# Kernel tuning notes

Hardware: AMD Instinct MI355X
Metric: run time of the kernel (lower is better)

## Reference

```python
import jax, jax.numpy as jnp
import numpy as np

B, N, D, R, E = 512, 32, 300, 5, 256
V_SENSE, V_GLOBAL = 20000, 50000  # last_idx_senses, last_idx_globals - last_idx_senses


def setup_inputs() -> dict:
    key = jax.random.key(0)
    ks = jax.random.split(key, 10)
    x = jax.random.normal(ks[0], (B, N, D), jnp.float32)
    edge_index = jax.random.randint(ks[1], (B, 2, E), 0, N)
    edge_type = jnp.sort(jax.random.randint(ks[2], (B, E), 0, R), axis=-1)
    # parameters (xavier-ish scales)
    conv_W = jax.random.normal(ks[3], (R, D, D), jnp.float32) * np.float32(1.0 / np.sqrt(D))
    W0 = jax.random.normal(ks[4], (D, D), jnp.float32) * np.float32(np.sqrt(2.0 / (D + D)))
    update_gate = jnp.ones((1,), jnp.float32)
    glob_W = jax.random.normal(ks[5], (V_GLOBAL, D), jnp.float32) * np.float32(1.0 / np.sqrt(D))
    glob_b = jnp.zeros((V_GLOBAL,), jnp.float32)
    sense_W = jax.random.normal(ks[6], (V_SENSE, D), jnp.float32) * np.float32(1.0 / np.sqrt(D))
    sense_b = jnp.zeros((V_SENSE,), jnp.float32)
    memory0 = jnp.zeros((N, D), jnp.float32)  # initial persisted memory (zeros vector broadcast)
    return dict(x=x, edge_index=edge_index, edge_type=edge_type, conv_W=conv_W, W0=W0,
                update_gate=update_gate, glob_W=glob_W, glob_b=glob_b,
                sense_W=sense_W, sense_b=sense_b, memory0=memory0)


def reference(x, edge_index, edge_type, conv_W, W0, update_gate, glob_W, glob_b, sense_W, sense_b, memory0):
    R_ = conv_W.shape[0]
    N_ = x.shape[1]

    def step(mem, inp):
        xs, ei, et = inp                      # [N,D], [2,E], [E]
        src, dst = ei[0], ei[1]
        # per-relation transformed features (GCNConv, bias=False)
        xw = jnp.einsum('nd,rde->rne', xs, conv_W)          # [R,N,D]
        # per-relation degrees with self-loops (PyG GCNConv symmetric norm)
        onehot = jax.nn.one_hot(et, R_, dtype=xs.dtype)     # [E,R]
        deg = 1.0 + jax.ops.segment_sum(onehot, dst, num_segments=N_)  # [N,R]
        dinv = jax.lax.rsqrt(deg)                           # [N,R]
        coeff = dinv[src, et] * dinv[dst, et]               # [E]
        msg = coeff[:, None] * xw[et, src]                  # [E,D]
        agg = jax.ops.segment_sum(msg, dst, num_segments=N_)  # sum over relations' convs
        self_term = jnp.einsum('rnd,nr->nd', xw, dinv * dinv)  # self-loop of each GCNConv
        composite = agg + self_term
        # prevlayer_connection = eye(N) @ (x @ W_0) = x @ W_0
        proposed = composite + xs @ W0
        new_mem = update_gate * proposed + (1.0 - update_gate) * mem  # rgcn_conv, persisted
        x1 = jax.nn.relu(new_mem)[0]                        # current node features [D]
        return new_mem, x1

    _, x1_all = jax.lax.scan(step, memory0, (x, edge_index, edge_type))  # [B,D]
    logits_g = x1_all @ glob_W.T + glob_b                   # [B,V_GLOBAL]
    logits_s = x1_all @ sense_W.T + sense_b                 # [B,V_SENSE]
    return (jax.nn.log_softmax(logits_g, axis=-1), jax.nn.log_softmax(logits_s, axis=-1))
```

## Files before the change

kernel.cpp:

```cpp
#include <hip/hip_runtime.h>
#include <stdint.h>

#define BDIM   512
#define NNODE  32
#define DDIM   300
#define NREL   5
#define NEDGE  256
#define VGLOB  50000
#define VSENSE 20000

#define K1PAD  1856
#define K2PAD  320
#define TG_GLOB  391
#define TG_SENSE 157
#define TGTOT  548
#define GROWS  50048
#define SROWS  20096
#define WROWS  70144
#define NCHUNK 3
#define KCH    10
#define NSCH   16
#define SCHL   32

#define NB_W2  5480
#define NB_Z   512
#define NB_W   2784

typedef __attribute__((ext_vector_type(8))) short short8;
typedef __attribute__((ext_vector_type(4))) float f32x4;
typedef _Float16 half_t;
typedef __attribute__((ext_vector_type(4))) _Float16 h16x4;

__device__ __forceinline__ unsigned short f2bf(float x) {
    unsigned int u = __float_as_uint(x);
    u += 0x7fffu + ((u >> 16) & 1u);
    return (unsigned short)(u >> 16);
}

__device__ __forceinline__ float powi(float x, int n) {
    float r = 1.f, p = x;
    while (n) { if (n & 1) r *= p; p *= p; n >>= 1; }
    return r;
}

#define AS1 __attribute__((address_space(1)))
#define AS3 __attribute__((address_space(3)))
__device__ __forceinline__ void gload16(const void* gp, void* lp) {
    __builtin_amdgcn_global_load_lds((AS1 void*)gp, (AS3 void*)lp, 16, 0, 0);
}

__global__ __launch_bounds__(256) void k_prep_all(
    const float* __restrict__ x, const int* __restrict__ ei,
    const int* __restrict__ et, unsigned short* __restrict__ Zb,
    const float* __restrict__ convW, const float* __restrict__ W0f,
    unsigned short* __restrict__ Wcb,
    const float* __restrict__ globW, const float* __restrict__ senseW,
    unsigned short* __restrict__ Wgb, int zbase)
{
    int blk = blockIdx.x, t = threadIdx.x;

    if (blk < zbase) {
        int idx = blk * 256 + t;
        int row = idx / 20, q0 = (idx - row * 20) * 4;
        const float* srcp = nullptr;
        if (row < GROWS) { if (row < VGLOB) srcp = globW + (size_t)row * DDIM; }
        else { int sr = row - GROWS; if (sr < VSENSE) srcp = senseW + (size_t)sr * DDIM; }
        unsigned int pk[8];
#pragma unroll
        for (int j = 0; j < 4; j++) {
            int kq = (q0 + j) * 4;
            unsigned int p0 = 0, p1 = 0;
            if (srcp && kq < DDIM) {
                float4 v = *(const float4*)(srcp + kq);
                p0 = (unsigned int)f2bf(v.x) | ((unsigned int)f2bf(v.y) << 16);
                p1 = (unsigned int)f2bf(v.z) | ((unsigned int)f2bf(v.w) << 16);
            }
            pk[2 * j] = p0; pk[2 * j + 1] = p1;
        }
        uint4* dst = (uint4*)(Wgb + (size_t)row * K2PAD + q0 * 4);
        uint4 u0; u0.x = pk[0]; u0.y = pk[1]; u0.z = pk[2]; u0.w = pk[3];
        uint4 u1; u1.x = pk[4]; u1.y = pk[5]; u1.z = pk[6]; u1.w = pk[7];
        dst[0] = u0; dst[1] = u1;
        return;
    }

    if (blk < zbase + NB_Z) {
        int b = blk - zbase;
        __shared__ int   cnt[NNODE * NREL];
        __shared__ float dinv[NNODE * NREL];
        __shared__ int   ssrc[NEDGE];
        __shared__ int   sdst[NEDGE];
        __shared__ int   setp[NEDGE];
        __shared__ float z[6][DDIM];

        const int* src = ei + (size_t)b * 2 * NEDGE;
        const int* dst = src + NEDGE;
        const int* etb = et + (size_t)b * NEDGE;

        if (t < NNODE * NREL) cnt[t] = 0;
        __syncthreads();
        if (t < NEDGE) {
            int s = src[t], d = dst[t], r = etb[t];
            ssrc[t] = s; sdst[t] = d; setp[t] = r;
            atomicAdd(&cnt[d * NREL + r], 1);
        }
        __syncthreads();
        if (t < NNODE * NREL) dinv[t] = rsqrtf(1.0f + (float)cnt[t]);
        __syncthreads();

        const float* xb = x + (size_t)b * NNODE * DDIM;
        for (int d = t; d < DDIM; d += 256) {
            float x0 = xb[d];
#pragma unroll
            for (int r = 0; r < NREL; r++) { float c = dinv[r]; z[r][d] = c * c * x0; }
            z[5][d] = x0;
        }
        __syncthreads();
        for (int e = 0; e < NEDGE; e++) {
            if (sdst[e] != 0) continue;
            int s = ssrc[e], r = setp[e];
            float coeff = dinv[s * NREL + r] * dinv[r];
            const float* xs = xb + (size_t)s * DDIM;
            for (int d = t; d < DDIM; d += 256) z[r][d] += coeff * xs[d];
        }
        __syncthreads();
        unsigned short* zo = Zb + (size_t)b * K1PAD;
        for (int k = t; k < K1PAD; k += 256) {
            unsigned short v = 0;
            if (k < 6 * DDIM) { int r = k / DDIM, d = k - r * DDIM; v = f2bf(z[r][d]); }
            zo[k] = v;
        }
        return;
    }

    {
        int idx = (blk - zbase - NB_Z) * 256 + t;
        if (idx >= 384 * K1PAD) return;
        int n = idx / K1PAD, k = idx - n * K1PAD;
        float v = 0.f;
        if (n < DDIM && k < 6 * DDIM) {
            int r = k / DDIM, d = k - r * DDIM;
            v = (r < NREL) ? convW[((size_t)r * DDIM + d) * DDIM + n]
                           : W0f[(size_t)d * DDIM + n];
        }
        Wcb[idx] = f2bf(v);
    }
}

template<int MODE, bool ST16>
__global__ __launch_bounds__(256) void k_gemm_b(
    const unsigned short* __restrict__ A, int ldk, int nk, int kchunk,
    int tiles0,
    const unsigned short* __restrict__ B0, int ldb0,
    const float* __restrict__ bias0, void* __restrict__ C0v, long ldc0,
    int nstore0, int tilebase0,
    const unsigned short* __restrict__ B1, int ldb1,
    const float* __restrict__ bias1, void* __restrict__ C1v, long ldc1,
    int nstore1, int tilebase1,
    float* __restrict__ pmax, float* __restrict__ psum)
{
    __shared__ __align__(16) char Alds[128 * 128];
    __shared__ __align__(16) char Blds[128 * 128];

    int t = threadIdx.x;
    int tile, mrep;
    if constexpr (MODE == 0) {
        tile = blockIdx.x; mrep = blockIdx.y;
    } else {
        int i = blockIdx.x + TGTOT * blockIdx.y;
        if (i < 2176) { int g = i >> 5, r = i & 31; tile = g * 8 + (r & 7); mrep = r >> 3; }
        else          { int j = i - 2176; tile = 544 + (j & 3); mrep = j >> 2; }
    }

    const unsigned short* Bp; const float* bias; void* Coutv;
    long ldc; int ldb, nstore, tileidx, tloc;
    if (tile < tiles0) {
        Bp = B0; bias = bias0; Coutv = C0v; ldc = ldc0;
        ldb = ldb0; nstore = nstore0; tloc = tile; tileidx = tilebase0 + tile;
    } else {
        tloc = tile - tiles0;
        Bp = B1; bias = bias1; Coutv = C1v; ldc = ldc1;
        ldb = ldb1; nstore = nstore1; tileidx = tilebase1 + tloc;
    }
    int n0 = tloc * 128;
    int m0 = mrep * 128;

    int kt_lo = 0, kt_hi = nk >> 6;
    float* Cf = (float*)Coutv;
    if constexpr (MODE == 0) {
        if (kchunk > 0) {
            kt_lo = blockIdx.z * kchunk;
            int hi = kt_lo + kchunk;
            if (hi < kt_hi) kt_hi = hi;
            Cf += (size_t)blockIdx.z * (BDIM * 304);
        }
    }

    int lane = t & 63, wid = t >> 6;
    int wm = wid >> 1, wn = wid & 1;
    int l15 = lane & 15, lq = lane >> 4;

    int trow = t >> 3;
    int sb = ((t & 7) << 4) ^ ((trow & 7) << 4);
    const char* Ag = (const char*)A + (size_t)(m0 + trow) * (ldk * 2) + sb;
    const char* Bg = (const char*)Bp + (size_t)(n0 + trow) * (ldb * 2) + sb;
    char* Al = Alds + t * 16;
    char* Bl = Blds + t * 16;
    size_t a32 = (size_t)32 * (ldk * 2);
    size_t b32 = (size_t)32 * (ldb * 2);

    int sw = (l15 & 7) << 4;
    int aoff0 = (lq * 16) ^ sw;
    int aoff1 = (64 + lq * 16) ^ sw;
    const char* Arow = Alds + (wm * 64 + l15) * 128;
    const char* Brow = Blds + (wn * 64 + l15) * 128;

    f32x4 acc[4][4] = {};

    for (int kt = kt_lo; kt < kt_hi; ++kt) {
        int k0b = kt << 7;
        const char* Agk = Ag + k0b;
        const char* Bgk = Bg + k0b;
#pragma unroll
        for (int c = 0; c < 4; c++) {
            gload16(Agk + c * a32, Al + c * 4096);
            gload16(Bgk + c * b32, Bl + c * 4096);
        }
        __syncthreads();
        short8 afr[4][2], bfr[4][2];
#pragma unroll
        for (int i = 0; i < 4; i++) {
            const char* Ab = Arow + i * (16 * 128);
            const char* Bb = Brow + i * (16 * 128);
            afr[i][0] = *(const short8*)(Ab + aoff0);
            afr[i][1] = *(const short8*)(Ab + aoff1);
            bfr[i][0] = *(const short8*)(Bb + aoff0);
            bfr[i][1] = *(const short8*)(Bb + aoff1);
        }
#pragma unroll
        for (int ks = 0; ks < 2; ks++)
#pragma unroll
            for (int mi = 0; mi < 4; mi++)
#pragma unroll
                for (int ni = 0; ni < 4; ni++)
                    acc[mi][ni] = __builtin_amdgcn_mfma_f32_16x16x32_bf16(
                        afr[mi][ks], bfr[ni][ks], acc[mi][ni], 0, 0, 0);
        __syncthreads();
    }

    if constexpr (MODE == 1) {
        half_t* Ch = (half_t*)Coutv;
        __shared__ float sMax[128][2];
        __shared__ float sSum[128][2];
#pragma unroll
        for (int mi = 0; mi < 4; mi++) {
            int row = m0 + wm * 64 + mi * 16 + lq * 4;
#pragma unroll
            for (int r = 0; r < 4; r++) {
                float vals[4];
                float rowmax = -3.0e38f;
#pragma unroll
                for (int ni = 0; ni < 4; ni++) {
                    int col = n0 + wn * 64 + ni * 16 + l15;
                    float v = -3.0e38f;
                    if (col < nstore) v = acc[mi][ni][r] + bias[col];
                    vals[ni] = v;
                    rowmax = fmaxf(rowmax, v);
                }
#pragma unroll
                for (int ni = 0; ni < 4; ni++) {
                    int col = n0 + wn * 64 + ni * 16 + l15;
                    if (col < nstore) {
                        if constexpr (ST16)
                            Ch[(size_t)(row + r) * ldc + col] = (half_t)vals[ni];
                        else
                            Cf[(size_t)(row + r) * ldc + col] = vals[ni];
                    }
                }
#pragma unroll
                for (int off = 1; off < 16; off <<= 1)
                    rowmax = fmaxf(rowmax, __shfl_xor(rowmax, off, 64));
                float s = 0.f;
#pragma unroll
                for (int ni = 0; ni < 4; ni++) s += __expf(vals[ni] - rowmax);
#pragma unroll
                for (int off = 1; off < 16; off <<= 1) s += __shfl_xor(s, off, 64);
                if (l15 == 0) {
                    int rl = wm * 64 + mi * 16 + lq * 4 + r;
                    sMax[rl][wn] = rowmax; sSum[rl][wn] = s;
                }
            }
        }
        __syncthreads();
        if (t < 128) {
            float ma = sMax[t][0], mb = sMax[t][1];
            float M = fmaxf(ma, mb);
            float S = sSum[t][0] * __expf(ma - M) + sSum[t][1] * __expf(mb - M);
            size_t o = (size_t)tileidx * BDIM + (m0 + t);
            pmax[o] = M; psum[o] = S;
        }
    } else {
#pragma unroll
        for (int mi = 0; mi < 4; mi++) {
            int row = m0 + wm * 64 + mi * 16 + lq * 4;
#pragma unroll
            for (int ni = 0; ni < 4; ni++) {
                int col = n0 + wn * 64 + ni * 16 + l15;
                if (col < 304) {
#pragma unroll
                    for (int r = 0; r < 4; r++)
                        Cf[(size_t)(row + r) * ldc + col] = acc[mi][ni][r];
                }
            }
        }
    }
}

__global__ __launch_bounds__(256) void k_gemm_f32(
    const unsigned short* __restrict__ A, int ldk, int nk,
    int tiles0,
    const float* __restrict__ B0, int ldb0, int ksrc0, int brows0,
    const float* __restrict__ bias0, float* __restrict__ C0, long ldc0,
    int nstore0, int tilebase0,
    const float* __restrict__ B1, int ldb1, int ksrc1, int brows1,
    const float* __restrict__ bias1, float* __restrict__ C1, long ldc1,
    int nstore1, int tilebase1,
    float* __restrict__ pmax, float* __restrict__ psum)
{
    __shared__ __align__(16) short Alds[128 * 32];
    __shared__ __align__(16) short Blds[128 * 32];

    int t = threadIdx.x;
    int bx = blockIdx.x;
    const float* Bsrc; const float* bias; float* Cout;
    long ldc; int ldb, ksrc, brows, nstore, tileidx;
    if (bx < tiles0) {
        Bsrc = B0; bias = bias0; Cout = C0; ldc = ldc0;
        ldb = ldb0; ksrc = ksrc0; brows = brows0; nstore = nstore0;
        tileidx = tilebase0 + bx;
    } else {
        bx -= tiles0;
        Bsrc = B1; bias = bias1; Cout = C1; ldc = ldc1;
        ldb = ldb1; ksrc = ksrc1; brows = brows1; nstore = nstore1;
        tileidx = tilebase1 + bx;
    }
    int n0 = bx * 128;
    int m0 = blockIdx.y * 128;

    int lane = t & 63, wid = t >> 6;
    int wm = wid >> 1, wn = wid & 1;
    int l15 = lane & 15, lq = lane >> 4;

    f32x4 acc[4][4] = {};

    int arow = t >> 1, acol = (t & 1) * 16;
    const unsigned short* aptr = A + (size_t)(m0 + arow) * ldk + acol;
    int brow = t >> 3, bkq = (t & 7) * 4;

    int kt_hi = nk / 32;
    for (int kt = 0; kt < kt_hi; ++kt) {
        int k0 = kt * 32;
        uint4 a0 = *(const uint4*)(aptr + k0);
        uint4 a1 = *(const uint4*)(aptr + k0 + 8);
        float4 bv[4];
#pragma unroll
        for (int j = 0; j < 4; j++) {
            int row = n0 + brow + 32 * j;
            float4 v = {0.f, 0.f, 0.f, 0.f};
            if (row < brows && (k0 + bkq + 4) <= ksrc)
                v = *(const float4*)(Bsrc + (size_t)row * ldb + k0 + bkq);
            bv[j] = v;
        }
        __syncthreads();
        *(uint4*)&Alds[arow * 32 + acol] = a0;
        *(uint4*)&Alds[arow * 32 + acol + 8] = a1;
#pragma unroll
        for (int j = 0; j < 4; j++) {
            unsigned int p0 = (unsigned int)f2bf(bv[j].x) | ((unsigned int)f2bf(bv[j].y) << 16);
            unsigned int p1 = (unsigned int)f2bf(bv[j].z) | ((unsigned int)f2bf(bv[j].w) << 16);
            uint2 pp; pp.x = p0; pp.y = p1;
            *(uint2*)&Blds[(brow + 32 * j) * 32 + bkq] = pp;
        }
        __syncthreads();
        short8 afr[4], bfr[4];
#pragma unroll
        for (int i = 0; i < 4; i++) {
            afr[i] = *(const short8*)&Alds[(wm * 64 + i * 16 + l15) * 32 + lq * 8];
            bfr[i] = *(const short8*)&Blds[(wn * 64 + i * 16 + l15) * 32 + lq * 8];
        }
#pragma unroll
        for (int mi = 0; mi < 4; mi++)
#pragma unroll
            for (int ni = 0; ni < 4; ni++)
                acc[mi][ni] = __builtin_amdgcn_mfma_f32_16x16x32_bf16(
                    afr[mi], bfr[ni], acc[mi][ni], 0, 0, 0);
    }

    __shared__ float sMax[128][2];
    __shared__ float sSum[128][2];
#pragma unroll
    for (int mi = 0; mi < 4; mi++) {
        int row = m0 + wm * 64 + mi * 16 + lq * 4;
#pragma unroll
        for (int r = 0; r < 4; r++) {
            float vals[4];
            float rowmax = -3.0e38f;
#pragma unroll
            for (int ni = 0; ni < 4; ni++) {
                int col = n0 + wn * 64 + ni * 16 + l15;
                float v = -3.0e38f;
                if (col < nstore) v = acc[mi][ni][r] + bias[col];
                vals[ni] = v;
                rowmax = fmaxf(rowmax, v);
            }
#pragma unroll
            for (int ni = 0; ni < 4; ni++) {
                int col = n0 + wn * 64 + ni * 16 + l15;
                if (col < nstore) Cout[(size_t)(row + r) * ldc + col] = vals[ni];
            }
#pragma unroll
            for (int off = 1; off < 16; off <<= 1)
                rowmax = fmaxf(rowmax, __shfl_xor(rowmax, off, 64));
            float s = 0.f;
#pragma unroll
            for (int ni = 0; ni < 4; ni++) s += __expf(vals[ni] - rowmax);
#pragma unroll
            for (int off = 1; off < 16; off <<= 1) s += __shfl_xor(s, off, 64);
            if (l15 == 0) {
                int rl = wm * 64 + mi * 16 + lq * 4 + r;
                sMax[rl][wn] = rowmax; sSum[rl][wn] = s;
            }
        }
    }
    __syncthreads();
    if (t < 128) {
        float ma = sMax[t][0], mb = sMax[t][1];
        float M = fmaxf(ma, mb);
        float S = sSum[t][0] * __expf(ma - M) + sSum[t][1] * __expf(mb - M);
        size_t o = (size_t)tileidx * BDIM + (m0 + t);
        pmax[o] = M; psum[o] = S;
    }
}

__global__ __launch_bounds__(320) void k_scan_local(
    const float* __restrict__ prop, float* __restrict__ scanA,
    const float* __restrict__ gate)
{
    int d = threadIdx.x; if (d >= 304) return;
    int blk = blockIdx.x;
    float g = gate[0], og = 1.f - g;
    float m = 0.f;
    const float* p0 = prop + (size_t)blk * SCHL * 304 + d;
    const float* p1 = p0 + (size_t)BDIM * 304;
    const float* p2 = p1 + (size_t)BDIM * 304;
    float* o = scanA + (size_t)blk * SCHL * 304 + d;
#pragma unroll
    for (int i = 0; i < SCHL; i++) {
        size_t off = (size_t)i * 304;
        float pv = p0[off] + p1[off] + p2[off];
        m = g * pv + og * m;
        o[off] = m;
    }
}

__global__ __launch_bounds__(320) void k_finalize_x1(
    const float* __restrict__ scanA, const float* __restrict__ mem0,
    const float* __restrict__ gate, unsigned short* __restrict__ x1b)
{
    int b = blockIdx.x, d = threadIdx.x;
    unsigned short v = 0;
    if (d < DDIM) {
        float g = gate[0], og = 1.f - g;
        float cS = powi(og, SCHL);
        int chunk = b >> 5;
        float m = mem0[d];
        for (int c = 0; c < chunk; c++)
            m = scanA[(size_t)(c * SCHL + SCHL - 1) * 304 + d] + cS * m;
        float mval = scanA[(size_t)b * 304 + d]
                   + powi(og, (b & (SCHL - 1)) + 1) * m;
        v = f2bf(fmaxf(mval, 0.f));
    }
    if (d < K2PAD) x1b[(size_t)b * K2PAD + d] = v;
}

template<bool F16L>
__global__ __launch_bounds__(256) void k_lse_fix(
    const float* __restrict__ pmax, const float* __restrict__ psum,
    const half_t* __restrict__ Lbuf, float* __restrict__ out)
{
    int b = blockIdx.x, seg = blockIdx.y, t = threadIdx.x;
    int base = seg ? TG_GLOB : 0;
    int nt = seg ? TG_SENSE : TG_GLOB;
    float M = -3.0e38f, S = 0.f;
    for (int i = t; i < nt; i += 256) {
        size_t o = (size_t)(base + i) * BDIM + b;
        float m = pmax[o], s = psum[o];
        if (m > M) { S = S * __expf(M - m) + s; M = m; }
        else       { S += s * __expf(m - M); }
    }
#pragma unroll
    for (int off = 1; off < 64; off <<= 1) {
        float Mo = __shfl_xor(M, off, 64), So = __shfl_xor(S, off, 64);
        float Mn = fmaxf(M, Mo);
        S = S * __expf(M - Mn) + So * __expf(Mo - Mn);
        M = Mn;
    }
    __shared__ float sM[4], sS[4];
    __shared__ float sL;
    int lane = t & 63, wid = t >> 6;
    if (lane == 0) { sM[wid] = M; sS[wid] = S; }
    __syncthreads();
    if (t == 0) {
        M = sM[0]; S = sS[0];
#pragma unroll
        for (int w = 1; w < 4; w++) {
            float Mo = sM[w], So = sS[w];
            float Mn = fmaxf(M, Mo);
            S = S * __expf(M - Mn) + So * __expf(Mo - Mn);
            M = Mn;
        }
        sL = M + __logf(S);
    }
    __syncthreads();
    float L = sL;
    float* orow = seg ? out + (size_t)BDIM * VGLOB + (size_t)b * VSENSE
                      : out + (size_t)b * VGLOB;
    int n4 = (seg ? VSENSE : VGLOB) >> 2;
    if constexpr (F16L) {
        const half_t* lrow = seg ? Lbuf + (size_t)BDIM * VGLOB + (size_t)b * VSENSE
                                 : Lbuf + (size_t)b * VGLOB;
        for (int i = t; i < n4; i += 256) {
            h16x4 hv = *(const h16x4*)(lrow + (size_t)i * 4);
            float4 v;
            v.x = (float)hv[0] - L; v.y = (float)hv[1] - L;
            v.z = (float)hv[2] - L; v.w = (float)hv[3] - L;
            ((float4*)orow)[i] = v;
        }
    } else {
        float4* r4 = (float4*)orow;
        for (int i = t; i < n4; i += 256) {
            float4 v = r4[i];
            v.x -= L; v.y -= L; v.z -= L; v.w -= L;
            r4[i] = v;
        }
    }
}

extern "C" void kernel_launch(void* const* d_in, const int* in_sizes, int n_in,
                              void* d_out, int out_size, void* d_ws, size_t ws_size,
                              hipStream_t stream)
{
    (void)in_sizes; (void)n_in; (void)out_size;
    const float* x      = (const float*)d_in[0];
    const int*   ei     = (const int*)d_in[1];
    const int*   et     = (const int*)d_in[2];
    const float* convW  = (const float*)d_in[3];
    const float* W0f    = (const float*)d_in[4];
    const float* gate   = (const float*)d_in[5];
    const float* globW  = (const float*)d_in[6];
    const float* globB  = (const float*)d_in[7];
    const float* senseW = (const float*)d_in[8];
    const float* senseB = (const float*)d_in[9];
    const float* mem0   = (const float*)d_in[10];
    float* out = (float*)d_out;

    char* w = (char*)d_ws;
    unsigned short* Zb  = (unsigned short*)(w + 0);
    unsigned short* Wcb = (unsigned short*)(w + 1900544);
    unsigned short* x1b = (unsigned short*)(w + 3325952);
    float* prop         = (float*)(w + 3653632);
    float* scanA        = (float*)(w + 5521408);
    float* pmax         = (float*)(w + 6144000);
    float* psum         = (float*)(w + 7266304);
    unsigned short* Wgb = (unsigned short*)(w + 8388608);
    half_t* Lbuf        = (half_t*)(w + 53280768);
    const size_t WS_NEED_BIG = 53280768;
    const size_t WS_NEED_L   = 53280768 + (size_t)BDIM * (VGLOB + VSENSE) * 2;
    bool bigws = ws_size >= WS_NEED_BIG;
    bool lws   = ws_size >= WS_NEED_L;

    int zbase = bigws ? NB_W2 : 0;
    int nprep = zbase + NB_Z + NB_W;
    k_prep_all<<<nprep, 256, 0, stream>>>(x, ei, et, Zb, convW, W0f, Wcb,
                                          globW, senseW, Wgb, zbase);

    k_gemm_b<0, false><<<dim3(3, 4, NCHUNK), 256, 0, stream>>>(Zb, K1PAD, K1PAD, KCH,
        3, Wcb, K1PAD, nullptr, (void*)prop, 304, 304, 0,
        nullptr, 0, nullptr, nullptr, 0, 0, 0,
        nullptr, nullptr);

    k_scan_local<<<NSCH, 320, 0, stream>>>(prop, scanA, gate);
    k_finalize_x1<<<BDIM, 320, 0, stream>>>(scanA, mem0, gate, x1b);

    if (bigws) {
        const unsigned short* WgbS = Wgb + (size_t)GROWS * K2PAD;
        if (lws) {
            k_gemm_b<1, true><<<dim3(TGTOT, 4), 256, 0, stream>>>(x1b, K2PAD, K2PAD, 0,
                TG_GLOB, Wgb, K2PAD, globB, (void*)Lbuf, VGLOB, VGLOB, 0,
                WgbS, K2PAD, senseB, (void*)(Lbuf + (size_t)BDIM * VGLOB), VSENSE, VSENSE, TG_GLOB,
                pmax, psum);
            k_lse_fix<true><<<dim3(BDIM, 2), 256, 0, stream>>>(pmax, psum, Lbuf, out);
        } else {
            k_gemm_b<1, false><<<dim3(TGTOT, 4), 256, 0, stream>>>(x1b, K2PAD, K2PAD, 0,
                TG_GLOB, Wgb, K2PAD, globB, (void*)out, VGLOB, VGLOB, 0,
                WgbS, K2PAD, senseB, (void*)(out + (size_t)BDIM * VGLOB), VSENSE, VSENSE, TG_GLOB,
                pmax, psum);
            k_lse_fix<false><<<dim3(BDIM, 2), 256, 0, stream>>>(pmax, psum, nullptr, out);
        }
    } else {
        k_gemm_f32<<<dim3(TGTOT, 4), 256, 0, stream>>>(x1b, K2PAD, K2PAD,
            TG_GLOB, globW, DDIM, DDIM, VGLOB, globB, out, VGLOB, VGLOB, 0,
            senseW, DDIM, DDIM, VSENSE, senseB, out + (size_t)BDIM * VGLOB, VSENSE, VSENSE, TG_GLOB,
            pmax, psum);
        k_lse_fix<false><<<dim3(BDIM, 2), 256, 0, stream>>>(pmax, psum, nullptr, out);
    }
}
```

Baseline: 410.6 us.

## Stage fp16 logits in upper half of output rows instead of separate workspace

The GEMM now writes fp16 logits into the second half of each fp32 output row, and the log-softmax fix pass reads them back in place and expands them to fp32. This removes the separate large Lbuf workspace, so the fp16 path no longer depends on a very large workspace size. A block-wide sync between read and write is needed so that no thread overwrites fp16 values another thread has not yet read. The weight conversion prep is also rewritten with one float4 per thread using four times as many blocks, for finer-grained coalescing.

```diff
diff --git a/kernel.cpp b/kernel.cpp
--- a/kernel.cpp
+++ b/kernel.cpp
@@ -22,7 +22,7 @@
 #define NSCH   16
 #define SCHL   32
 
-#define NB_W2  5480
+#define NB_W2  21920
 #define NB_Z   512
 #define NB_W   2784
 
@@ -61,26 +61,20 @@
 
     if (blk < zbase) {
         int idx = blk * 256 + t;
-        int row = idx / 20, q0 = (idx - row * 20) * 4;
-        const float* srcp = nullptr;
-        if (row < GROWS) { if (row < VGLOB) srcp = globW + (size_t)row * DDIM; }
-        else { int sr = row - GROWS; if (sr < VSENSE) srcp = senseW + (size_t)sr * DDIM; }
-        unsigned int pk[8];
-#pragma unroll
-        for (int j = 0; j < 4; j++) {
-            int kq = (q0 + j) * 4;
-            unsigned int p0 = 0, p1 = 0;
-            if (srcp && kq < DDIM) {
+        int row = idx / 80, kq = (idx - row * 80) * 4;
+        unsigned int p0 = 0, p1 = 0;
+        if (kq < DDIM) {
+            const float* srcp = nullptr;
+            if (row < GROWS) { if (row < VGLOB) srcp = globW + (size_t)row * DDIM; }
+            else { int sr = row - GROWS; if (sr < VSENSE) srcp = senseW + (size_t)sr * DDIM; }
+            if (srcp) {
                 float4 v = *(const float4*)(srcp + kq);
                 p0 = (unsigned int)f2bf(v.x) | ((unsigned int)f2bf(v.y) << 16);
                 p1 = (unsigned int)f2bf(v.z) | ((unsigned int)f2bf(v.w) << 16);
             }
-            pk[2 * j] = p0; pk[2 * j + 1] = p1;
-        }
-        uint4* dst = (uint4*)(Wgb + (size_t)row * K2PAD + q0 * 4);
-        uint4 u0; u0.x = pk[0]; u0.y = pk[1]; u0.z = pk[2]; u0.w = pk[3];
-        uint4 u1; u1.x = pk[4]; u1.y = pk[5]; u1.z = pk[6]; u1.w = pk[7];
-        dst[0] = u0; dst[1] = u1;
+        }
+        uint2 pp; pp.x = p0; pp.y = p1;
+        *(uint2*)(Wgb + (size_t)row * K2PAD + kq) = pp;
         return;
     }
 
@@ -249,7 +243,6 @@
     }
 
     if constexpr (MODE == 1) {
-        half_t* Ch = (half_t*)Coutv;
         __shared__ float sMax[128][2];
         __shared__ float sSum[128][2];
 #pragma unroll
@@ -267,13 +260,19 @@
                     vals[ni] = v;
                     rowmax = fmaxf(rowmax, v);
                 }
-#pragma unroll
-                for (int ni = 0; ni < 4; ni++) {
-                    int col = n0 + wn * 64 + ni * 16 + l15;
-                    if (col < nstore) {
-                        if constexpr (ST16)
-                            Ch[(size_t)(row + r) * ldc + col] = (half_t)vals[ni];
-                        else
+                if constexpr (ST16) {
+                    half_t* hrow = (half_t*)((char*)Coutv
+                                 + (size_t)(row + r) * (ldc * 4) + ldc * 2);
+#pragma unroll
+                    for (int ni = 0; ni < 4; ni++) {
+                        int col = n0 + wn * 64 + ni * 16 + l15;
+                        if (col < nstore) hrow[col] = (half_t)vals[ni];
+                    }
+                } else {
+#pragma unroll
+                    for (int ni = 0; ni < 4; ni++) {
+                        int col = n0 + wn * 64 + ni * 16 + l15;
+                        if (col < nstore)
                             Cf[(size_t)(row + r) * ldc + col] = vals[ni];
                     }
                 }
@@ -486,7 +485,7 @@
 template<bool F16L>
 __global__ __launch_bounds__(256) void k_lse_fix(
     const float* __restrict__ pmax, const float* __restrict__ psum,
-    const half_t* __restrict__ Lbuf, float* __restrict__ out)
+    float* __restrict__ out)
 {
     int b = blockIdx.x, seg = blockIdx.y, t = threadIdx.x;
     int base = seg ? TG_GLOB : 0;
@@ -523,18 +522,24 @@
     }
     __syncthreads();
     float L = sL;
+    int nseg = seg ? VSENSE : VGLOB;
     float* orow = seg ? out + (size_t)BDIM * VGLOB + (size_t)b * VSENSE
                       : out + (size_t)b * VGLOB;
-    int n4 = (seg ? VSENSE : VGLOB) >> 2;
+    int n4 = nseg >> 2;
     if constexpr (F16L) {
-        const half_t* lrow = seg ? Lbuf + (size_t)BDIM * VGLOB + (size_t)b * VSENSE
-                                 : Lbuf + (size_t)b * VGLOB;
-        for (int i = t; i < n4; i += 256) {
-            h16x4 hv = *(const h16x4*)(lrow + (size_t)i * 4);
-            float4 v;
-            v.x = (float)hv[0] - L; v.y = (float)hv[1] - L;
-            v.z = (float)hv[2] - L; v.w = (float)hv[3] - L;
-            ((float4*)orow)[i] = v;
+        const half_t* lrow = (const half_t*)((const char*)orow + (size_t)nseg * 2);
+        int niter = (n4 + 255) >> 8;
+        for (int k = 0; k < niter; k++) {
+            int i = (k << 8) + t;
+            h16x4 hv = {};
+            if (i < n4) hv = *(const h16x4*)(lrow + (size_t)i * 4);
+            __syncthreads();
+            if (i < n4) {
+                float4 v;
+                v.x = (float)hv[0] - L; v.y = (float)hv[1] - L;
+                v.z = (float)hv[2] - L; v.w = (float)hv[3] - L;
+                ((float4*)orow)[i] = v;
+            }
         }
     } else {
         float4* r4 = (float4*)orow;
@@ -573,11 +578,8 @@
     float* pmax         = (float*)(w + 6144000);
     float* psum         = (float*)(w + 7266304);
     unsigned short* Wgb = (unsigned short*)(w + 8388608);
-    half_t* Lbuf        = (half_t*)(w + 53280768);
-    const size_t WS_NEED_BIG = 53280768;
-    const size_t WS_NEED_L   = 53280768 + (size_t)BDIM * (VGLOB + VSENSE) * 2;
+    const size_t WS_NEED_BIG = 8388608 + (size_t)WROWS * K2PAD * 2;
     bool bigws = ws_size >= WS_NEED_BIG;
-    bool lws   = ws_size >= WS_NEED_L;
 
     int zbase = bigws ? NB_W2 : 0;
     int nprep = zbase + NB_Z + NB_W;
@@ -594,24 +596,16 @@
 
     if (bigws) {
         const unsigned short* WgbS = Wgb + (size_t)GROWS * K2PAD;
-        if (lws) {
-            k_gemm_b<1, true><<<dim3(TGTOT, 4), 256, 0, stream>>>(x1b, K2PAD, K2PAD, 0,
-                TG_GLOB, Wgb, K2PAD, globB, (void*)Lbuf, VGLOB, VGLOB, 0,
-                WgbS, K2PAD, senseB, (void*)(Lbuf + (size_t)BDIM * VGLOB), VSENSE, VSENSE, TG_GLOB,
-                pmax, psum);
-            k_lse_fix<true><<<dim3(BDIM, 2), 256, 0, stream>>>(pmax, psum, Lbuf, out);
-        } else {
-            k_gemm_b<1, false><<<dim3(TGTOT, 4), 256, 0, stream>>>(x1b, K2PAD, K2PAD, 0,
-                TG_GLOB, Wgb, K2PAD, globB, (void*)out, VGLOB, VGLOB, 0,
-                WgbS, K2PAD, senseB, (void*)(out + (size_t)BDIM * VGLOB), VSENSE, VSENSE, TG_GLOB,
-                pmax, psum);
-            k_lse_fix<false><<<dim3(BDIM, 2), 256, 0, stream>>>(pmax, psum, nullptr, out);
-        }
+        k_gemm_b<1, true><<<dim3(TGTOT, 4), 256, 0, stream>>>(x1b, K2PAD, K2PAD, 0,
+            TG_GLOB, Wgb, K2PAD, globB, (void*)out, VGLOB, VGLOB, 0,
+            WgbS, K2PAD, senseB, (void*)(out + (size_t)BDIM * VGLOB), VSENSE, VSENSE, TG_GLOB,
+            pmax, psum);
+        k_lse_fix<true><<<dim3(BDIM, 2), 256, 0, stream>>>(pmax, psum, out);
     } else {
         k_gemm_f32<<<dim3(TGTOT, 4), 256, 0, stream>>>(x1b, K2PAD, K2PAD,
             TG_GLOB, globW, DDIM, DDIM, VGLOB, globB, out, VGLOB, VGLOB, 0,
             senseW, DDIM, DDIM, VSENSE, senseB, out + (size_t)BDIM * VGLOB, VSENSE, VSENSE, TG_GLOB,
             pmax, psum);
-        k_lse_fix<false><<<dim3(BDIM, 2), 256, 0, stream>>>(pmax, psum, nullptr, out);
-    }
-}
+        k_lse_fix<false><<<dim3(BDIM, 2), 256, 0, stream>>>(pmax, psum, out);
+    }
+}
```

After: 390.9 us. -4.8%, faster.
